# Performance work log

Hardware: AMD Instinct MI355X
Metric: run time of the kernel (lower is better)

Reference implementation:

```python
import jax, jax.numpy as jnp
import numpy as np

# init constants (match init_kwargs)
NGH, SUB_Q, SUB_D, POS_D, NEG_D, BORDER, SUB_D_NEG = 7, 8, 1, 2, 4, 16, 8
BATCH_STRIDE = 512.0  # hardcoded `b * 512` offset in the original cdist call


def _offsets():
    # faithful port of NghSampler.precompute_offsets
    rad = (NGH // SUB_D) * NGH
    pos, neg = [], []
    for j in range(-rad, rad + 1, SUB_D):
        for i in range(-rad, rad + 1, SUB_D):
            d2 = i * i + j * j
            if d2 <= POS_D ** 2:
                pos.append((i, j))
            elif NEG_D ** 2 <= d2 <= NGH ** 2:
                neg.append((i, j))
    return np.array(pos, np.int32).T, np.array(neg, np.int32).T  # [2,P],[2,Nn]


def _grid(step, B, H, W):
    # gen_grid with step > 0: regular grid inside the border, flattened
    xs = np.arange(BORDER, W - BORDER, step)
    ys = np.arange(BORDER, H - BORDER, step)
    H1, W1 = len(ys), len(xs)
    b = np.repeat(np.arange(B), H1 * W1)
    y = np.tile(np.repeat(ys, W1), B)
    x = np.tile(np.tile(xs, H1), B)
    return b, y, x, (B, H1, W1)


def setup_inputs() -> dict:
    key = jax.random.key(0)
    B, D, H, W = 2, 128, 512, 512
    k1, k2, k3, k4, k5 = jax.random.split(key, 5)
    pos_off, neg_off = _offsets()
    return {
        "feat1": jax.random.normal(k1, (B, D, H, W), jnp.float32),
        "feat2": jax.random.normal(k2, (B, D, H, W), jnp.float32),
        "conf1": jax.random.uniform(k3, (B, 1, H, W), jnp.float32),
        "conf2": jax.random.uniform(k4, (B, 1, H, W), jnp.float32),
        # dense flow: target (x, y) coords in image 2, a few out of bounds
        "aflow": jax.random.uniform(k5, (B, 2, H, W), jnp.float32, -10.0, W + 10.0),
        "pos_offsets": jnp.asarray(pos_off),
        "neg_offsets": jnp.asarray(neg_off),
    }


def reference(feat1, feat2, conf1, conf2, aflow, pos_offsets, neg_offsets):
    B, two, H, W = aflow.shape
    b1, y1, x1, shape = _grid(SUB_Q, B, H, W)      # n = B*H1*W1 query points

    f1 = feat1[b1, :, y1, x1]                      # [n, D]
    qconf = conf1[b1, 0, y1, x1].reshape(shape)    # (B, H1, W1)

    # (aflow + 0.5).long(): truncation toward zero, as torch .long()
    xy2 = jnp.transpose(aflow[b1, :, y1, x1] + 0.5).astype(jnp.int32)  # [2, n]
    mask = ((xy2[0] >= 0) & (xy2[1] >= 0) & (xy2[0] < W) & (xy2[1] < H)).reshape(shape)

    def clamp(xy):
        return jnp.stack([jnp.clip(xy[0], 0, W - 1), jnp.clip(xy[1], 0, H - 1)])

    # positive ring: gather feat2 at offset pixels -> [P, n, D], dot with f1
    xy2p = clamp(xy2[:, None, :] + pos_offsets[:, :, None])  # [2, P, n]
    pscores = jnp.einsum('nk,pnk->np', f1, feat2[b1, :, xy2p[1], xy2p[0]])
    # negative ring -> [Nn, n, D]
    xy2n = clamp(xy2[:, None, :] + neg_offsets[:, :, None])  # [2, Nn, n]
    nscores = jnp.einsum('nk,ink->ni', f1, feat2[b1, :, xy2n[1], xy2n[0]])

    # distractors: regular grid over image 2
    b3, y3, x3, _ = _grid(SUB_D_NEG, B, H, W)      # n3 points
    d3 = feat2[b3, :, y3, x3]                      # [n3, D]
    dscores = jnp.einsum('nk,ik->ni', f1, d3)      # [n, n3]

    # cdist with per-batch 512 offset (un-clamped xy2, as in the original)
    qx = xy2[0].astype(jnp.float32) + BATCH_STRIDE * b1
    qy = xy2[1].astype(jnp.float32) + BATCH_STRIDE * b1
    dx = x3.astype(np.float32) + BATCH_STRIDE * b3
    dy = y3.astype(np.float32) + BATCH_STRIDE * b3
    dis = jnp.sqrt((qx[:, None] - dx[None, :]) ** 2 + (qy[:, None] - dy[None, :]) ** 2)
    dscores = jnp.where(dis < NEG_D, 0.0, dscores)

    scores = jnp.concatenate([pscores, nscores, dscores], axis=1)
    n, P = pscores.shape
    gt = jnp.concatenate([jnp.ones((n, P), jnp.uint8),
                          jnp.zeros((n, scores.shape[1] - P), jnp.uint8)], axis=1)
    return scores, gt, mask, qconf
```

## Files before the change

### kernel.cpp

```cpp
#include <hip/hip_runtime.h>
#include <hip/hip_bf16.h>
#include <stdint.h>

#define B_ 2
#define D_ 128
#define H_ 512
#define W_ 512
#define G_ 60
#define NQ_ 7200
#define BORDER_ 16
#define STEP_ 8

typedef __attribute__((ext_vector_type(8))) short short8;
typedef __attribute__((ext_vector_type(4))) float f32x4;
typedef __attribute__((ext_vector_type(4))) uint32_t u32x4;

__device__ __forceinline__ float bf_lo(uint32_t u){ return __builtin_bit_cast(float, u << 16); }
__device__ __forceinline__ float bf_hi(uint32_t u){ return __builtin_bit_cast(float, u & 0xffff0000u); }

__device__ __forceinline__ uint32_t pack2bf(float lo, float hi){
  uint16_t l = __builtin_bit_cast(uint16_t, __float2bfloat16(lo));
  uint16_t h = __builtin_bit_cast(uint16_t, __float2bfloat16(hi));
  return (uint32_t)l | ((uint32_t)h << 16);
}

__global__ __launch_bounds__(256) void gtzero_k(f32x4* __restrict__ gt, size_t n4){
  size_t i = (size_t)blockIdx.x * 256 + threadIdx.x;
  size_t stride = (size_t)gridDim.x * 256;
  f32x4 z = {0.f, 0.f, 0.f, 0.f};
  for (; i < n4; i += stride)
    __builtin_nontemporal_store(z, gt + i);
}

__global__ __launch_bounds__(256) void transpose_k(const float* __restrict__ src,
                                                   __hip_bfloat16* __restrict__ dst){
  __shared__ uint32_t lds2[64][65];
  int b = blockIdx.z, y = blockIdx.y, x0 = blockIdx.x * 64;
  int tid = threadIdx.x;
  size_t plane = (size_t)H_ * W_;

  int xq = tid & 15;
  int eg = tid >> 4;
  size_t base_in = (((size_t)b * D_) * H_ + y) * W_ + x0 + 4 * xq;
  #pragma unroll
  for (int it = 0; it < 4; ++it){
    int e = eg + 16 * it;
    f32x4 lo = __builtin_nontemporal_load(
        reinterpret_cast<const f32x4*>(src + base_in + (size_t)(2 * e) * plane));
    f32x4 hi = __builtin_nontemporal_load(
        reinterpret_cast<const f32x4*>(src + base_in + (size_t)(2 * e + 1) * plane));
    lds2[e][4 * xq + 0] = pack2bf(lo[0], hi[0]);
    lds2[e][4 * xq + 1] = pack2bf(lo[1], hi[1]);
    lds2[e][4 * xq + 2] = pack2bf(lo[2], hi[2]);
    lds2[e][4 * xq + 3] = pack2bf(lo[3], hi[3]);
  }
  __syncthreads();

  int eq = tid & 15;
  int xb = tid >> 4;
  size_t pixbase = (((size_t)b * H_ + y) * W_ + x0);
  #pragma unroll
  for (int it = 0; it < 4; ++it){
    int x = xb + 16 * it;
    u32x4 v;
    v[0] = lds2[4 * eq + 0][x];
    v[1] = lds2[4 * eq + 1][x];
    v[2] = lds2[4 * eq + 2][x];
    v[3] = lds2[4 * eq + 3][x];
    *reinterpret_cast<u32x4*>(dst + (pixbase + x) * D_ + 8 * eq) = v;
  }
}

template<bool USE_T>
__global__ __launch_bounds__(128) void prep_k(
    const float* __restrict__ feat1, const float* __restrict__ feat2,
    const __hip_bfloat16* __restrict__ f2t,
    const float* __restrict__ conf1, const float* __restrict__ aflow,
    __hip_bfloat16* __restrict__ f1o, __hip_bfloat16* __restrict__ d3o,
    float2* __restrict__ qxy, float2* __restrict__ dxy,
    float* __restrict__ omask, float* __restrict__ oqconf)
{
  int n = blockIdx.x;
  int b = n / (G_ * G_); int r = n % (G_ * G_);
  int iy = r / G_, ix = r % G_;
  int y1 = BORDER_ + iy * STEP_, x1 = BORDER_ + ix * STEP_;
  int tid = threadIdx.x;
  size_t pix = ((size_t)b * H_ + y1) * W_ + x1;
  if (tid < 64){
    int d = tid * 2;
    size_t o = (((size_t)b * D_ + d) * H_ + y1) * W_ + x1;
    float lo = feat1[o];
    float hi = feat1[o + (size_t)H_ * W_];
    *reinterpret_cast<uint32_t*>(f1o + (size_t)n * D_ + d) = pack2bf(lo, hi);
    if (tid == 0){
      float ax = aflow[(((size_t)b * 2 + 0) * H_ + y1) * W_ + x1];
      float ay = aflow[(((size_t)b * 2 + 1) * H_ + y1) * W_ + x1];
      int x2 = (int)(ax + 0.5f);
      int y2 = (int)(ay + 0.5f);
      omask[n] = (x2 >= 0 && y2 >= 0 && x2 < W_ && y2 < H_) ? 1.0f : 0.0f;
      oqconf[n] = conf1[pix];
      float bs = 512.0f * (float)b;
      qxy[n] = make_float2((float)x2 + bs, (float)y2 + bs);
      dxy[n] = make_float2((float)x1 + bs, (float)y1 + bs);
    }
  } else {
    int d = (tid - 64) * 2;
    uint32_t u;
    if (USE_T){
      u = *reinterpret_cast<const uint32_t*>(f2t + pix * D_ + d);
    } else {
      size_t o = (((size_t)b * D_ + d) * H_ + y1) * W_ + x1;
      u = pack2bf(feat2[o], feat2[o + (size_t)H_ * W_]);
    }
    *reinterpret_cast<uint32_t*>(d3o + (size_t)n * D_ + d) = u;
  }
}

template<bool USE_T>
__global__ __launch_bounds__(256) void posneg_k(
    const __hip_bfloat16* __restrict__ f1o,
    const __hip_bfloat16* __restrict__ f2t,
    const float* __restrict__ feat2,
    const float* __restrict__ aflow,
    const int* __restrict__ pos, const int* __restrict__ neg,
    int P, int NN, float* __restrict__ out, int NCOL, size_t GTOFF)
{
  int n = blockIdx.x;
  int b = n / (G_ * G_); int r = n % (G_ * G_);
  int iy = r / G_, ix = r % G_;
  int y1 = BORDER_ + iy * STEP_, x1 = BORDER_ + ix * STEP_;
  int tid = threadIdx.x;
  int l16 = tid & 15, grp = tid >> 4;

  const uint4 av = *reinterpret_cast<const uint4*>(f1o + (size_t)n * D_ + l16 * 8);
  float a[8];
  a[0] = bf_lo(av.x); a[1] = bf_hi(av.x); a[2] = bf_lo(av.y); a[3] = bf_hi(av.y);
  a[4] = bf_lo(av.z); a[5] = bf_hi(av.z); a[6] = bf_lo(av.w); a[7] = bf_hi(av.w);

  float ax = aflow[(((size_t)b * 2 + 0) * H_ + y1) * W_ + x1];
  float ay = aflow[(((size_t)b * 2 + 1) * H_ + y1) * W_ + x1];
  int x2 = (int)(ax + 0.5f), y2 = (int)(ay + 0.5f);

  int NP = P + NN;
  for (int p0 = 0; p0 < NP; p0 += 16){
    int p = p0 + grp;
    float s = 0.0f;
    if (p < NP){
      int ox, oy;
      if (p < P){ ox = pos[p]; oy = pos[P + p]; }
      else      { ox = neg[p - P]; oy = neg[NN + p - P]; }
      int px = min(max(x2 + ox, 0), W_ - 1);
      int py = min(max(y2 + oy, 0), H_ - 1);
      if (USE_T){
        const uint4 v = *reinterpret_cast<const uint4*>(
            f2t + (((size_t)b * H_ + py) * W_ + px) * D_ + l16 * 8);
        s = a[0]*bf_lo(v.x) + a[1]*bf_hi(v.x) + a[2]*bf_lo(v.y) + a[3]*bf_hi(v.y)
          + a[4]*bf_lo(v.z) + a[5]*bf_hi(v.z) + a[6]*bf_lo(v.w) + a[7]*bf_hi(v.w);
      } else {
        size_t o = (((size_t)b * D_ + l16 * 8) * H_ + py) * W_ + px;
        #pragma unroll
        for (int j = 0; j < 8; ++j) s += a[j] * feat2[o + (size_t)j * H_ * W_];
      }
    }
    s += __shfl_xor(s, 1); s += __shfl_xor(s, 2);
    s += __shfl_xor(s, 4); s += __shfl_xor(s, 8);
    if (p < NP && l16 == 0){
      size_t idx = (size_t)n * NCOL + p;
      out[idx] = s;
      out[GTOFF + idx] = (p < P) ? 1.0f : 0.0f;
    }
  }
}

__global__ __launch_bounds__(256) void gemm_k(
    const __hip_bfloat16* __restrict__ f1o, const __hip_bfloat16* __restrict__ d3o,
    const float2* __restrict__ qxy, const float2* __restrict__ dxy,
    float* __restrict__ out, int NCOL, int CB)
{
  __shared__ float sT[4][16][100];
  int m0 = blockIdx.x * 16;
  int tid = threadIdx.x;
  int lane = tid & 63, wid = tid >> 6;
  int r16 = lane & 15, kg = lane >> 4;

  int c = blockIdx.y * 4 + wid;
  int cn0 = c * 64;
  int nc = (c == 111) ? 96 : 64;

  short8 af[4];
  #pragma unroll
  for (int ks = 0; ks < 4; ++ks)
    af[ks] = *reinterpret_cast<const short8*>(
        f1o + (size_t)(m0 + r16) * D_ + ks * 32 + kg * 8);

  f32x4 acc[6] = {};
  #pragma unroll
  for (int j = 0; j < 6; ++j){
    if (j * 16 < nc){
      int nn = cn0 + j * 16 + r16;
      #pragma unroll
      for (int ks = 0; ks < 4; ++ks){
        short8 br = *reinterpret_cast<const short8*>(
            d3o + (size_t)nn * D_ + ks * 32 + kg * 8);
        acc[j] = __builtin_amdgcn_mfma_f32_16x16x32_bf16(br, af[ks], acc[j], 0, 0, 0);
      }
    }
  }

  #pragma unroll
  for (int j = 0; j < 6; ++j)
    if (j * 16 < nc)
      *reinterpret_cast<f32x4*>(&sT[wid][r16][j * 16 + kg * 4]) = acc[j];

  float2 dcA = dxy[cn0 + lane];
  float2 dcB = dxy[cn0 + ((nc > 64) ? 64 + (lane & 31) : lane)];

  #pragma unroll
  for (int r = 0; r < 16; ++r){
    int m = m0 + r;
    float2 q = qxy[m];
    size_t S = (size_t)m * NCOL + CB + cn0;
    float v = sT[wid][r][lane];
    float ddx = q.x - dcA.x, ddy = q.y - dcA.y;
    out[S + lane] = (ddx * ddx + ddy * ddy < 16.0f) ? 0.0f : v;
    if (nc > 64 && lane < 32){
      float v2 = sT[wid][r][64 + lane];
      float ddx2 = q.x - dcB.x, ddy2 = q.y - dcB.y;
      out[S + 64 + lane] = (ddx2 * ddx2 + ddy2 * ddy2 < 16.0f) ? 0.0f : v2;
    }
  }
}

extern "C" void kernel_launch(void* const* d_in, const int* in_sizes, int n_in,
                              void* d_out, int out_size, void* d_ws, size_t ws_size,
                              hipStream_t stream)
{
  const float* feat1 = (const float*)d_in[0];
  const float* feat2 = (const float*)d_in[1];
  const float* conf1 = (const float*)d_in[2];
  const float* aflow = (const float*)d_in[4];
  const int* pos = (const int*)d_in[5];
  const int* neg = (const int*)d_in[6];
  int P = in_sizes[5] / 2, NN = in_sizes[6] / 2;
  int NCOL = P + NN + NQ_;
  size_t GTOFF = (size_t)NQ_ * (size_t)NCOL;
  float* out = (float*)d_out;

  char* ws = (char*)d_ws;
  __hip_bfloat16* f1o = (__hip_bfloat16*)ws;
  __hip_bfloat16* d3o = (__hip_bfloat16*)(ws + 1843200);
  float2* qxy = (float2*)(ws + 3686400);
  float2* dxy = (float2*)(ws + 3744000);
  __hip_bfloat16* f2t = (__hip_bfloat16*)(ws + 3801600);
  size_t needT = 3801600ull + (size_t)B_ * H_ * W_ * D_ * 2;
  bool useT = ws_size >= needT;

  float* omask  = out + 2 * GTOFF;
  float* oqconf = omask + NQ_;

  gtzero_k<<<2048, 256, 0, stream>>>((f32x4*)(out + GTOFF), GTOFF / 4);

  if (useT){
    transpose_k<<<dim3(W_ / 64, H_, B_), 256, 0, stream>>>(feat2, f2t);
    prep_k<true><<<NQ_, 128, 0, stream>>>(feat1, feat2, f2t, conf1, aflow,
                                          f1o, d3o, qxy, dxy, omask, oqconf);
    posneg_k<true><<<NQ_, 256, 0, stream>>>(f1o, f2t, feat2, aflow, pos, neg,
                                            P, NN, out, NCOL, GTOFF);
  } else {
    prep_k<false><<<NQ_, 128, 0, stream>>>(feat1, feat2, f2t, conf1, aflow,
                                           f1o, d3o, qxy, dxy, omask, oqconf);
    posneg_k<false><<<NQ_, 256, 0, stream>>>(f1o, f2t, feat2, aflow, pos, neg,
                                             P, NN, out, NCOL, GTOFF);
  }
  gemm_k<<<dim3(NQ_ / 16, 28), 256, 0, stream>>>(f1o, d3o, qxy, dxy,
                                                 out, NCOL, P + NN);
}
```

Before: 302.8 us.

## Widen gemm column spans, fuse distance mask, and emit aligned nontemporal vector stores

Each wave in the distractor GEMM kernel now covers 256 columns instead of 64. The distance mask is applied in registers right after the MFMA, and results are staged in shared memory shifted so each output row can be written with 16-byte-aligned nontemporal vector stores plus scalar head and tail stores. The GEMM launch is also moved before the pos/neg kernel. The aim is to cut the store-bound cost of writing the large score matrix, at the price of more shared memory per block and some idle waves in the last block column.

```diff
diff --git a/kernel.cpp b/kernel.cpp
--- a/kernel.cpp
+++ b/kernel.cpp
@@ -177,15 +177,17 @@
     const float2* __restrict__ qxy, const float2* __restrict__ dxy,
     float* __restrict__ out, int NCOL, int CB)
 {
-  __shared__ float sT[4][16][100];
+  __shared__ float sT[4][16][264];
   int m0 = blockIdx.x * 16;
   int tid = threadIdx.x;
   int lane = tid & 63, wid = tid >> 6;
   int r16 = lane & 15, kg = lane >> 4;
 
-  int c = blockIdx.y * 4 + wid;
-  int cn0 = c * 64;
-  int nc = (c == 111) ? 96 : 64;
+  int span = blockIdx.y * 4 + wid;
+  if (span >= 29) return;
+  int c0 = span * 256;
+  int ncols = NQ_ - c0; if (ncols > 256) ncols = 256;
+  int nj = (ncols + 15) >> 4;
 
   short8 af[4];
   #pragma unroll
@@ -193,41 +195,55 @@
     af[ks] = *reinterpret_cast<const short8*>(
         f1o + (size_t)(m0 + r16) * D_ + ks * 32 + kg * 8);
 
-  f32x4 acc[6] = {};
-  #pragma unroll
-  for (int j = 0; j < 6; ++j){
-    if (j * 16 < nc){
-      int nn = cn0 + j * 16 + r16;
+  size_t Sr = (size_t)(m0 + r16) * NCOL + CB + c0;
+  int hme = (int)((4 - (Sr & 3)) & 3);
+  float2 q = qxy[m0 + r16];
+
+  #pragma unroll
+  for (int j = 0; j < 16; ++j){
+    if (j < nj){
+      int nn = c0 + j * 16 + r16;
+      f32x4 acc = {0.f, 0.f, 0.f, 0.f};
       #pragma unroll
       for (int ks = 0; ks < 4; ++ks){
         short8 br = *reinterpret_cast<const short8*>(
             d3o + (size_t)nn * D_ + ks * 32 + kg * 8);
-        acc[j] = __builtin_amdgcn_mfma_f32_16x16x32_bf16(br, af[ks], acc[j], 0, 0, 0);
+        acc = __builtin_amdgcn_mfma_f32_16x16x32_bf16(br, af[ks], acc, 0, 0, 0);
       }
-    }
-  }
-
-  #pragma unroll
-  for (int j = 0; j < 6; ++j)
-    if (j * 16 < nc)
-      *reinterpret_cast<f32x4*>(&sT[wid][r16][j * 16 + kg * 4]) = acc[j];
-
-  float2 dcA = dxy[cn0 + lane];
-  float2 dcB = dxy[cn0 + ((nc > 64) ? 64 + (lane & 31) : lane)];
-
-  #pragma unroll
+      int nb0 = c0 + j * 16 + kg * 4;
+      f32x4 d01 = *reinterpret_cast<const f32x4*>(dxy + nb0);
+      f32x4 d23 = *reinterpret_cast<const f32x4*>(dxy + nb0 + 2);
+      float ddx0 = q.x - d01[0], ddy0 = q.y - d01[1];
+      float ddx1 = q.x - d01[2], ddy1 = q.y - d01[3];
+      float ddx2 = q.x - d23[0], ddy2 = q.y - d23[1];
+      float ddx3 = q.x - d23[2], ddy3 = q.y - d23[3];
+      if (ddx0 * ddx0 + ddy0 * ddy0 < 16.0f) acc[0] = 0.0f;
+      if (ddx1 * ddx1 + ddy1 * ddy1 < 16.0f) acc[1] = 0.0f;
+      if (ddx2 * ddx2 + ddy2 * ddy2 < 16.0f) acc[2] = 0.0f;
+      if (ddx3 * ddx3 + ddy3 * ddy3 < 16.0f) acc[3] = 0.0f;
+      int base = 4 + j * 16 + kg * 4 - hme;
+      sT[wid][r16][base + 0] = acc[0];
+      sT[wid][r16][base + 1] = acc[1];
+      sT[wid][r16][base + 2] = acc[2];
+      sT[wid][r16][base + 3] = acc[3];
+    }
+  }
+
+  #pragma unroll 1
   for (int r = 0; r < 16; ++r){
-    int m = m0 + r;
-    float2 q = qxy[m];
-    size_t S = (size_t)m * NCOL + CB + cn0;
-    float v = sT[wid][r][lane];
-    float ddx = q.x - dcA.x, ddy = q.y - dcA.y;
-    out[S + lane] = (ddx * ddx + ddy * ddy < 16.0f) ? 0.0f : v;
-    if (nc > 64 && lane < 32){
-      float v2 = sT[wid][r][64 + lane];
-      float ddx2 = q.x - dcB.x, ddy2 = q.y - dcB.y;
-      out[S + 64 + lane] = (ddx2 * ddx2 + ddy2 * ddy2 < 16.0f) ? 0.0f : v2;
-    }
+    size_t S = (size_t)(m0 + r) * NCOL + CB + c0;
+    int h = (int)((4 - (S & 3)) & 3);
+    int nb = (ncols - h) >> 2;
+    const float* row = &sT[wid][r][0];
+    if (lane < nb){
+      f32x4 v = *reinterpret_cast<const f32x4*>(row + 4 + 4 * lane);
+      __builtin_nontemporal_store(v, reinterpret_cast<f32x4*>(out + S + h + 4 * lane));
+    }
+    if (lane < h)
+      __builtin_nontemporal_store(row[4 + lane - h], out + S + lane);
+    int t0 = h + nb * 4;
+    if (lane < ncols - t0)
+      __builtin_nontemporal_store(row[4 + t0 + lane - h], out + S + t0 + lane);
   }
 }
 
@@ -264,14 +280,16 @@
     transpose_k<<<dim3(W_ / 64, H_, B_), 256, 0, stream>>>(feat2, f2t);
     prep_k<true><<<NQ_, 128, 0, stream>>>(feat1, feat2, f2t, conf1, aflow,
                                           f1o, d3o, qxy, dxy, omask, oqconf);
+    gemm_k<<<dim3(NQ_ / 16, 8), 256, 0, stream>>>(f1o, d3o, qxy, dxy,
+                                                  out, NCOL, P + NN);
     posneg_k<true><<<NQ_, 256, 0, stream>>>(f1o, f2t, feat2, aflow, pos, neg,
                                             P, NN, out, NCOL, GTOFF);
   } else {
     prep_k<false><<<NQ_, 128, 0, stream>>>(feat1, feat2, f2t, conf1, aflow,
                                            f1o, d3o, qxy, dxy, omask, oqconf);
+    gemm_k<<<dim3(NQ_ / 16, 8), 256, 0, stream>>>(f1o, d3o, qxy, dxy,
+                                                  out, NCOL, P + NN);
     posneg_k<false><<<NQ_, 256, 0, stream>>>(f1o, f2t, feat2, aflow, pos, neg,
                                              P, NN, out, NCOL, GTOFF);
   }
-  gemm_k<<<dim3(NQ_ / 16, 28), 256, 0, stream>>>(f1o, d3o, qxy, dxy,
-                                                 out, NCOL, P + NN);
-}
+}
```

After: 310.5 us. 2.5% more time.
